# Kernel tuning notes

Measured on AMD Instinct MI355X. Metric: run time of the kernel, lower is better.

The kernel has to match this reference:

```python
import jax, jax.numpy as jnp
import numpy as np

HEADS, DIM_HEAD, DIM = 12, 64, 768
H = W = 32
N = H * W
B = 4


def _ln(x, g, b, eps=1e-5):
    mu = x.mean(-1, keepdims=True)
    var = ((x - mu) ** 2).mean(-1, keepdims=True)
    return (x - mu) / jnp.sqrt(var + eps) * g + b


def _get_epipolar(k, src_c2w, target_c2w, h=H, w=W):
    # Faithful port of Epipolar_Attention.get_epipolar, without the (hw*hw,3) repeat
    # materialization (uses broadcasting for the pairwise cross product instead).
    b = k.shape[0]
    Wf = h * 16.0 / 9.0
    k = k.astype(jnp.float32)
    k = k.at[:, 0, :].multiply(Wf).at[:, 1, :].multiply(float(h))
    k = k.at[:, 0, 2].set(h / 2.0).at[:, 1, 2].set(h / 2.0)
    ii, jj = jnp.meshgrid(jnp.arange(h), jnp.arange(w), indexing='ij')
    # after the torch column swap: (col, row, 1)
    coords = jnp.stack([jj.ravel(), ii.ravel(), jnp.ones(h * w, jnp.int32)], axis=1).astype(jnp.float32)  # [hw,3]
    k3 = k[:, :3, :3]
    src_r, src_t = src_c2w[:, :3, :3].astype(jnp.float32), src_c2w[:, :3, 3].astype(jnp.float32)
    tgt_r, tgt_t = target_c2w[:, :3, :3].astype(jnp.float32), target_c2w[:, :3, 3].astype(jnp.float32)
    tgt_rinv = jnp.linalg.inv(tgt_r)
    fx, fy = k3[:, 0, 0][:, None], k3[:, 1, 1][:, None]
    cx, cy = k3[:, 0, 2][:, None], k3[:, 1, 2][:, None]
    nc = jnp.stack([(coords[None, :, 0] - cx) / fx,
                    (coords[None, :, 1] - cy) / fy,
                    jnp.broadcast_to(coords[None, :, 2], (b, h * w))], axis=-1)  # [b,hw,3]
    p3w = jnp.einsum('bij,bnj->bni', src_r, nc) + src_t[:, None]
    p2 = jnp.einsum('bij,bnj->bni', tgt_rinv, p3w) - tgt_t[:, None]  # target_w2c_t = -target_c2w_t
    pij_un = jnp.einsum('bij,bnj->bni', k3, p2)                      # [b,hw,3]
    pij = pij_un / (pij_un[..., -1:] + 1e-6)
    o2 = jnp.einsum('bij,bj->bi', tgt_rinv, src_t) - tgt_t           # origin projected
    oij = jnp.einsum('bij,bj->bi', k3, o2)
    oij = oij / oij[..., -1:]
    oi_to_pi = pij - oij[:, None]                # [b,hw,3]
    oi_to_coord = coords[None] - oij[:, None]    # [b,hw,3]
    cr = jnp.cross(oi_to_pi[:, :, None, :], oi_to_coord[:, None, :, :])  # [b,hw,hw,3]
    area = jnp.sqrt((cr * cr).sum(-1))
    vlen = jnp.sqrt((oi_to_pi * oi_to_pi).sum(-1))[:, :, None]
    dist = area / vlen
    dw = 1.0 - jax.nn.sigmoid(50.0 * (dist - 0.5))
    row_max = dw.max(-1, keepdims=True)
    return jnp.where(row_max < 0.5, 1.0, dw)     # rows with max<0.5 are set to all-ones


def setup_inputs():
    key = jax.random.key(0)
    ks = jax.random.split(key, 16)
    s = 0.02
    x = jax.random.normal(ks[0], (B, N, DIM), jnp.float32)
    src_encode = jax.random.normal(ks[1], (B, N, DIM), jnp.float32)
    intrinsic = (jnp.zeros((B, 4, 4), jnp.float32)
                 .at[:, 0, 0].set(1.0).at[:, 1, 1].set(1.0)
                 .at[:, 0, 2].set(0.5).at[:, 1, 2].set(0.5)
                 .at[:, 2, 2].set(1.0).at[:, 3, 3].set(1.0))
    R = jnp.eye(3, dtype=jnp.float32) + 0.1 * jax.random.normal(ks[2], (2, B, 3, 3), jnp.float32)
    t = 0.5 * jax.random.normal(ks[3], (2, B, 3), jnp.float32)
    c2w = (jnp.zeros((2, B, 4, 4), jnp.float32)
           .at[:, :, :3, :3].set(R).at[:, :, :3, 3].set(t).at[:, :, 3, 3].set(1.0))
    hd = HEADS * DIM_HEAD
    w_ = lambda k_, shp: s * jax.random.normal(k_, shp, jnp.float32)
    return dict(
        x=x, src_encode=src_encode, intrinsic=intrinsic, c2w=c2w,
        lnq_g=jnp.ones(DIM), lnq_b=jnp.zeros(DIM), Wq=w_(ks[4], (DIM, hd)), bq=jnp.zeros(hd),
        lnk_g=jnp.ones(DIM), lnk_b=jnp.zeros(DIM), Wk=w_(ks[5], (DIM, hd)), bk=jnp.zeros(hd),
        lnv_g=jnp.ones(DIM), lnv_b=jnp.zeros(DIM), Wv=w_(ks[6], (DIM, hd)), bv=jnp.zeros(hd),
        Wp=w_(ks[7], (hd, DIM)), bp=jnp.zeros(DIM),
        pre_g=jnp.ones(DIM), pre_b=jnp.zeros(DIM),
        W1=w_(ks[8], (DIM, 2 * DIM)), b1=jnp.zeros(2 * DIM),
        W2=w_(ks[9], (2 * DIM, DIM)), b2=jnp.zeros(DIM),
        post_g=jnp.ones(DIM), post_b=jnp.zeros(DIM))


def reference(x, src_encode, intrinsic, c2w, lnq_g, lnq_b, Wq, bq, lnk_g, lnk_b, Wk, bk,
              lnv_g, lnv_b, Wv, bv, Wp, bp, pre_g, pre_b, W1, b1, W2, b2, post_g, post_b):
    b, n, _ = x.shape
    scale = DIM_HEAD ** -0.5
    split = lambda t_: t_.reshape(b, n, HEADS, DIM_HEAD).transpose(0, 2, 1, 3)  # [b,m,n,d]
    q = split(_ln(x, lnq_g, lnq_b) @ Wq + bq)
    k = split(_ln(src_encode, lnk_g, lnk_b) @ Wk + bk)
    v = split(_ln(src_encode, lnv_g, lnv_b) @ Wv + bv)
    scores = scale * jnp.einsum('bmqd,bmkd->bmqk', q, k)
    e1 = _get_epipolar(intrinsic, c2w[1], c2w[0])                    # do_epipolar
    e2 = jnp.swapaxes(_get_epipolar(intrinsic, c2w[0], c2w[1]), 1, 2)  # bidirectional (transposed)
    wmap = e1 * e2                                                   # [b,n,n], shared across heads
    att = jax.nn.softmax(scores * wmap[:, None], axis=-1)
    a = jnp.einsum('bmqk,bmkd->bmqd', att, v).transpose(0, 2, 1, 3).reshape(b, n, HEADS * DIM_HEAD)
    z = _ln(a @ Wp + bp, pre_g, pre_b)
    z = z + (jax.nn.gelu(z @ W1 + b1, approximate=False) @ W2 + b2)  # torch nn.GELU = exact erf
    z = _ln(z, post_g, post_b)
    wm_full = jnp.broadcast_to(wmap[:, None], (b, HEADS, n, n)).reshape(b * HEADS, n, n)
    return z, wm_full
```

## Files before the change

kernel.cpp:

```cpp
#include <hip/hip_runtime.h>
#include <hip/hip_bf16.h>

typedef unsigned short u16;
typedef __attribute__((ext_vector_type(4))) unsigned short u16x4;
typedef __attribute__((ext_vector_type(8))) unsigned short u16x8;
typedef __attribute__((ext_vector_type(8))) short s16x8;
typedef __attribute__((ext_vector_type(4))) float f32x4;

#define HEADS 12
#define NSEQ 1024
#define DIMM 768
#define DHEAD 64

__device__ __forceinline__ float b2f(u16 h) {
  union { unsigned u; float f; } v; v.u = ((unsigned)h) << 16; return v.f;
}
__device__ __forceinline__ u16 f2b(float f) {
  union { float f; unsigned u; } v; v.f = f;
  unsigned r = v.u + 0x7fffu + ((v.u >> 16) & 1u);
  return (u16)(r >> 16);
}
__device__ __forceinline__ void gl_lds16(const u16* g, u16* l) {
  __builtin_amdgcn_global_load_lds(
      (const __attribute__((address_space(1))) void*)g,
      (__attribute__((address_space(3))) void*)l, 16, 0, 0);
}

template<bool GELU, bool RESID>
__device__ __forceinline__ void gemm_body(
    const u16* __restrict__ A, const u16* __restrict__ BT,
    const float* __restrict__ bias, const u16* __restrict__ resid,
    const float* __restrict__ rg, const float* __restrict__ rb,
    u16* __restrict__ C, int K, int lda, int ldb, int ldc,
    int m0, int n0, u16* As, u16* Bs)
{
  const int tid = threadIdx.x;
  const int lane = tid & 63;
  const int wv = tid >> 6;
  const int wm0 = (wv >> 1) * 64;
  const int wn0 = (wv & 1) * 64;
  const int l15 = lane & 15;
  const int quad = lane >> 4;
  const int srow = lane >> 2;
  const int scol = (lane & 3) * 8;

  f32x4 acc[4][4];
  #pragma unroll
  for (int i = 0; i < 4; ++i)
    #pragma unroll
    for (int j = 0; j < 4; ++j)
      acc[i][j] = {0.f, 0.f, 0.f, 0.f};

  const u16* Ab = A + (long)(m0 + wv * 32 + srow) * lda + scol;
  const u16* Bb = BT + (long)(n0 + wv * 32 + srow) * ldb + scol;
  u16* AsW = As + (wv * 32) * 32;
  u16* BsW = Bs + (wv * 32) * 32;

  #pragma unroll
  for (int t = 0; t < 2; ++t) {
    gl_lds16(Ab + (long)t * 16 * lda, AsW + t * 16 * 32);
    gl_lds16(Bb + (long)t * 16 * ldb, BsW + t * 16 * 32);
  }

  int cur = 0;
  for (int k0 = 0; k0 < K; k0 += 32) {
    __syncthreads();
    if (k0 + 32 < K) {
      const int nxt = cur ^ 1;
      #pragma unroll
      for (int t = 0; t < 2; ++t) {
        gl_lds16(Ab + (k0 + 32) + (long)t * 16 * lda, AsW + nxt * 4096 + t * 16 * 32);
        gl_lds16(Bb + (k0 + 32) + (long)t * 16 * ldb, BsW + nxt * 4096 + t * 16 * 32);
      }
    }
    const u16* Ac = As + cur * 4096;
    const u16* Bc = Bs + cur * 4096;
    s16x8 af[4], bfr[4];
    #pragma unroll
    for (int i = 0; i < 4; ++i)
      af[i] = *(const s16x8*)&Ac[(wm0 + i * 16 + l15) * 32 + quad * 8];
    #pragma unroll
    for (int j = 0; j < 4; ++j)
      bfr[j] = *(const s16x8*)&Bc[(wn0 + j * 16 + l15) * 32 + quad * 8];
    #pragma unroll
    for (int i = 0; i < 4; ++i)
      #pragma unroll
      for (int j = 0; j < 4; ++j)
        acc[i][j] = __builtin_amdgcn_mfma_f32_16x16x32_bf16(af[i], bfr[j], acc[i][j], 0, 0, 0);
    cur ^= 1;
  }

  #pragma unroll
  for (int i = 0; i < 4; ++i)
    #pragma unroll
    for (int j = 0; j < 4; ++j) {
      const int col = n0 + wn0 + j * 16 + l15;
      const float bvv = bias[col];
      #pragma unroll
      for (int v = 0; v < 4; ++v) {
        const int row = m0 + wm0 + i * 16 + quad * 4 + v;
        float val = acc[i][j][v] + bvv;
        if (GELU) val = 0.5f * val * (1.0f + erff(val * 0.70710678118654752440f));
        if (RESID) val += b2f(resid[(long)row * ldc + col]) * rg[col] + rb[col];
        C[(long)row * ldc + col] = f2b(val);
      }
    }
}

template<bool GELU, bool RESID>
__global__ __launch_bounds__(256)
void gemm_one(const u16* __restrict__ A, const u16* __restrict__ BT,
              const float* __restrict__ bias, const u16* __restrict__ resid,
              const float* __restrict__ rg, const float* __restrict__ rb,
              u16* __restrict__ C, int K, int lda, int ldb, int ldc)
{
  __shared__ u16 As[8192], Bs[8192];
  gemm_body<GELU, RESID>(A, BT, bias, resid, rg, rb, C, K, lda, ldb, ldc,
                         blockIdx.x * 128, blockIdx.y * 128, As, Bs);
}

__global__ __launch_bounds__(256)
void gemm_qkv(const u16* __restrict__ nx, const u16* __restrict__ ns,
              const u16* __restrict__ qT, const u16* __restrict__ kvT,
              const float* __restrict__ bqf, const float* __restrict__ bkvf,
              u16* __restrict__ qb, u16* __restrict__ kvb)
{
  __shared__ u16 As[8192], Bs[8192];
  const int z = blockIdx.z;
  if (z == 0)
    gemm_body<false, false>(nx, qT, bqf, nullptr, nullptr, nullptr, qb,
                            768, 768, 768, 768,
                            blockIdx.x * 128, blockIdx.y * 128, As, Bs);
  else
    gemm_body<false, false>(ns, kvT, bkvf, nullptr, nullptr, nullptr, kvb,
                            768, 768, 768, 1536,
                            blockIdx.x * 128, (z - 1) * 768 + blockIdx.y * 128, As, Bs);
}

__global__ __launch_bounds__(256, 3)
void fattn(const u16* __restrict__ qb, const u16* __restrict__ kvb,
           const u16* __restrict__ vT, const u16* __restrict__ wm,
           u16* __restrict__ outA)
{
  __shared__ u16 Qs[2 * 64 * 32];
  __shared__ u16 Ks[2 * 64 * 32];
  __shared__ u16 Vs[2 * 64 * 32];
  __shared__ u16 Ws[64][72];
  __shared__ u16 Ps[64][72];

  const int bh = blockIdx.y;
  const int b = bh / HEADS, h = bh - b * HEADS;
  const int q0 = blockIdx.x * 64;
  const int tid = threadIdx.x;
  const int lane = tid & 63;
  const int wv = tid >> 6;
  const int l15 = lane & 15;
  const int quad = lane >> 4;
  const int srow = lane >> 2;
  const int scol = (lane & 3) * 8;

  const u16* Qg = qb + ((long)b * NSEQ + q0) * DIMM + h * DHEAD;
  const u16* Kg = kvb + (long)b * NSEQ * 1536 + h * DHEAD;
  const u16* Vg = vT + (long)bh * DHEAD * NSEQ;
  const u16* Wg = wm + ((long)b * NSEQ + q0) * NSEQ;

  #pragma unroll
  for (int h2 = 0; h2 < 2; ++h2)
    gl_lds16(Qg + (long)(wv * 16 + srow) * DIMM + h2 * 32 + scol,
             Qs + (h2 * 64 + wv * 16) * 32);

  f32x4 Sacc[4], Oacc[4];
  float mrow[4], lrow[4];
  #pragma unroll
  for (int j = 0; j < 4; ++j) {
    Oacc[j] = {0.f, 0.f, 0.f, 0.f};
    mrow[j] = -3.0e38f;
    lrow[j] = 0.f;
  }
  s16x8 qf[2];

  for (int kt = 0; kt < 16; ++kt) {
    __syncthreads();
    #pragma unroll
    for (int h2 = 0; h2 < 2; ++h2) {
      gl_lds16(Kg + (long)(kt * 64 + wv * 16 + srow) * 1536 + h2 * 32 + scol,
               Ks + (h2 * 64 + wv * 16) * 32);
      gl_lds16(Vg + (long)(wv * 16 + srow) * NSEQ + kt * 64 + h2 * 32 + scol,
               Vs + (h2 * 64 + wv * 16) * 32);
    }
    #pragma unroll
    for (int t = 0; t < 2; ++t) {
      const int col = (lane & 3) * 16 + t * 8;
      u16x8 wvv = *(const u16x8*)&Wg[(long)(wv * 16 + srow) * NSEQ + kt * 64 + col];
      *(u16x8*)&Ws[wv * 16 + srow][col] = wvv;
    }
    __syncthreads();

    if (kt == 0) {
      qf[0] = *(const s16x8*)&Qs[(0 * 64 + wv * 16 + l15) * 32 + quad * 8];
      qf[1] = *(const s16x8*)&Qs[(1 * 64 + wv * 16 + l15) * 32 + quad * 8];
    }

    #pragma unroll
    for (int j = 0; j < 4; ++j) Sacc[j] = {0.f, 0.f, 0.f, 0.f};
    #pragma unroll
    for (int j = 0; j < 4; ++j)
      #pragma unroll
      for (int h2 = 0; h2 < 2; ++h2) {
        s16x8 kf = *(const s16x8*)&Ks[(h2 * 64 + j * 16 + l15) * 32 + quad * 8];
        Sacc[j] = __builtin_amdgcn_mfma_f32_16x16x32_bf16(qf[h2], kf, Sacc[j], 0, 0, 0);
      }

    #pragma unroll
    for (int j = 0; j < 4; ++j)
      #pragma unroll
      for (int v = 0; v < 4; ++v)
        Sacc[j][v] *= b2f(Ws[wv * 16 + quad * 4 + v][j * 16 + l15]);
    #pragma unroll
    for (int v = 0; v < 4; ++v) {
      float tm = fmaxf(fmaxf(Sacc[0][v], Sacc[1][v]), fmaxf(Sacc[2][v], Sacc[3][v]));
      tm = fmaxf(tm, __shfl_xor(tm, 1));
      tm = fmaxf(tm, __shfl_xor(tm, 2));
      tm = fmaxf(tm, __shfl_xor(tm, 4));
      tm = fmaxf(tm, __shfl_xor(tm, 8));
      const float mnew = fmaxf(mrow[v], tm);
      const float al = __expf(mrow[v] - mnew);
      float rs = 0.f;
      #pragma unroll
      for (int j = 0; j < 4; ++j) {
        const float e = __expf(Sacc[j][v] - mnew);
        Sacc[j][v] = e;
        rs += e;
      }
      rs += __shfl_xor(rs, 1);
      rs += __shfl_xor(rs, 2);
      rs += __shfl_xor(rs, 4);
      rs += __shfl_xor(rs, 8);
      lrow[v] = lrow[v] * al + rs;
      mrow[v] = mnew;
      #pragma unroll
      for (int jn = 0; jn < 4; ++jn) Oacc[jn][v] *= al;
    }
    #pragma unroll
    for (int j = 0; j < 4; ++j)
      #pragma unroll
      for (int v = 0; v < 4; ++v)
        Ps[wv * 16 + quad * 4 + v][j * 16 + l15] = f2b(Sacc[j][v]);

    #pragma unroll
    for (int h2 = 0; h2 < 2; ++h2) {
      s16x8 af = *(const s16x8*)&Ps[wv * 16 + l15][h2 * 32 + quad * 8];
      #pragma unroll
      for (int jn = 0; jn < 4; ++jn) {
        s16x8 vf = *(const s16x8*)&Vs[(h2 * 64 + jn * 16 + l15) * 32 + quad * 8];
        Oacc[jn] = __builtin_amdgcn_mfma_f32_16x16x32_bf16(af, vf, Oacc[jn], 0, 0, 0);
      }
    }
  }

  #pragma unroll
  for (int v = 0; v < 4; ++v) {
    const int row = q0 + wv * 16 + quad * 4 + v;
    const float inv = 1.0f / lrow[v];
    #pragma unroll
    for (int jn = 0; jn < 4; ++jn)
      outA[((long)(b * NSEQ + row)) * DIMM + h * DHEAD + jn * 16 + l15] =
          f2b(Oacc[jn][v] * inv);
  }
}

template<bool F32IN>
__global__ __launch_bounds__(256)
void norm_k(const void* __restrict__ in, u16* __restrict__ out)
{
  const long base = (long)blockIdx.x * DIMM;
  const int tid = threadIdx.x;
  __shared__ float s1[8], s2[8];
  float v0, v1, v2;
  if (F32IN) {
    const float* p = (const float*)in + base;
    v0 = p[tid]; v1 = p[tid + 256]; v2 = p[tid + 512];
  } else {
    const u16* p = (const u16*)in + base;
    v0 = b2f(p[tid]); v1 = b2f(p[tid + 256]); v2 = b2f(p[tid + 512]);
  }
  float s = v0 + v1 + v2;
  #pragma unroll
  for (int off = 32; off; off >>= 1) s += __shfl_down(s, off);
  const int lane = tid & 63, wid = tid >> 6;
  if (!lane) s1[wid] = s;
  __syncthreads();
  if (!tid) s1[4] = s1[0] + s1[1] + s1[2] + s1[3];
  __syncthreads();
  const float mu = s1[4] / 768.0f;
  float d0 = v0 - mu, d1 = v1 - mu, d2 = v2 - mu;
  float sq = d0 * d0 + d1 * d1 + d2 * d2;
  #pragma unroll
  for (int off = 32; off; off >>= 1) sq += __shfl_down(sq, off);
  if (!lane) s2[wid] = sq;
  __syncthreads();
  if (!tid) s2[4] = s2[0] + s2[1] + s2[2] + s2[3];
  __syncthreads();
  const float rstd = 1.0f / sqrtf(s2[4] / 768.0f + 1e-5f);
  u16* o = out + base;
  o[tid]       = f2b(d0 * rstd);
  o[tid + 256] = f2b(d1 * rstd);
  o[tid + 512] = f2b(d2 * rstd);
}

__global__ __launch_bounds__(256)
void ln_final(const u16* __restrict__ in, const float* __restrict__ g,
              const float* __restrict__ bb, float* __restrict__ out)
{
  const long base = (long)blockIdx.x * DIMM;
  const int tid = threadIdx.x;
  __shared__ float s1[8], s2[8];
  const u16* p = in + base;
  float v0 = b2f(p[tid]), v1 = b2f(p[tid + 256]), v2 = b2f(p[tid + 512]);
  float s = v0 + v1 + v2;
  #pragma unroll
  for (int off = 32; off; off >>= 1) s += __shfl_down(s, off);
  const int lane = tid & 63, wid = tid >> 6;
  if (!lane) s1[wid] = s;
  __syncthreads();
  if (!tid) s1[4] = s1[0] + s1[1] + s1[2] + s1[3];
  __syncthreads();
  const float mu = s1[4] / 768.0f;
  float d0 = v0 - mu, d1 = v1 - mu, d2 = v2 - mu;
  float sq = d0 * d0 + d1 * d1 + d2 * d2;
  #pragma unroll
  for (int off = 32; off; off >>= 1) sq += __shfl_down(sq, off);
  if (!lane) s2[wid] = sq;
  __syncthreads();
  if (!tid) s2[4] = s2[0] + s2[1] + s2[2] + s2[3];
  __syncthreads();
  const float rstd = 1.0f / sqrtf(s2[4] / 768.0f + 1e-5f);
  float* o = out + base;
  o[tid]       = d0 * rstd * g[tid]       + bb[tid];
  o[tid + 256] = d1 * rstd * g[tid + 256] + bb[tid + 256];
  o[tid + 512] = d2 * rstd * g[tid + 512] + bb[tid + 512];
}

__global__ __launch_bounds__(256)
void trans_all(const float* w0, const float* w1, const float* w2,
               const float* w3, const float* w4, const float* w5,
               const float* gq, const float* gk, const float* gv, const float* gp,
               u16* d0, u16* d12, u16* d3, u16* d4, u16* d5)
{
  const float* src; const float* g; u16* dst; int R, C; float sc = 1.0f;
  switch (blockIdx.z) {
    case 0: src = w0; g = gq; dst = d0;  R = 768;  C = 768;  sc = 0.125f; break;
    case 1: src = w1; g = gk; dst = d12; R = 768;  C = 768;  break;
    case 2: src = w2; g = gv; dst = d12 + 768 * 768; R = 768; C = 768; break;
    case 3: src = w3; g = nullptr; dst = d3; R = 768;  C = 768;  break;
    case 4: src = w4; g = gp; dst = d4; R = 768;  C = 1536; break;
    default: src = w5; g = nullptr; dst = d5; R = 1536; C = 768; break;
  }
  const int c0 = blockIdx.x * 32;
  const int r0 = blockIdx.y * 32;
  if (c0 >= C || r0 >= R) return;
  __shared__ u16 t[32][36];
  const int tid = threadIdx.x;
  const int i = tid >> 3;
  const int j4 = (tid & 7) * 4;
  const float rs = (g ? g[r0 + i] : 1.0f) * sc;
  #pragma unroll
  for (int jj = 0; jj < 4; ++jj)
    t[i][j4 + jj] = f2b(src[(long)(r0 + i) * C + c0 + j4 + jj] * rs);
  __syncthreads();
  u16x4 ov;
  #pragma unroll
  for (int jj = 0; jj < 4; ++jj) ov[jj] = t[j4 + jj][i];
  *(u16x4*)&dst[(long)(c0 + i) * R + r0 + j4] = ov;
}

__global__ __launch_bounds__(256)
void biasfold(const float* Wq, const float* Wk, const float* Wv, const float* W1,
              const float* bq, const float* bk, const float* bv, const float* b1,
              const float* lnqb, const float* lnkb, const float* lnvb, const float* preb,
              float* obq, float* obkv, float* ob1)
{
  const int y = blockIdx.y;
  const int c = blockIdx.x * 256 + threadIdx.x;
  const float* W; const float* bln; const float* bw; float* out;
  int C; float sc = 1.0f;
  switch (y) {
    case 0: W = Wq; bln = lnqb; bw = bq; out = obq;        C = 768;  sc = 0.125f; break;
    case 1: W = Wk; bln = lnkb; bw = bk; out = obkv;       C = 768;  break;
    case 2: W = Wv; bln = lnvb; bw = bv; out = obkv + 768; C = 768;  break;
    default: W = W1; bln = preb; bw = b1; out = ob1;       C = 1536; break;
  }
  if (c >= C) return;
  float s = bw[c];
  for (int r = 0; r < 768; ++r) s += bln[r] * W[(long)r * C + c];
  out[c] = s * sc;
}

__global__ __launch_bounds__(256)
void v_transpose(const u16* __restrict__ kvb, u16* __restrict__ vT)
{
  __shared__ u16 t[64][72];
  const int z = blockIdx.y;
  const int b = z / HEADS, h = z - b * HEADS;
  const int n0 = blockIdx.x * 64;
  const int tid = threadIdx.x;
  const int i = tid >> 2;
  const int jb = (tid & 3) * 16;
  const u16* src = kvb + (long)(b * NSEQ + n0 + i) * 1536 + 768 + h * DHEAD + jb;
  *(u16x8*)&t[i][jb]     = *(const u16x8*)&src[0];
  *(u16x8*)&t[i][jb + 8] = *(const u16x8*)&src[8];
  __syncthreads();
  const int dd = tid >> 2;
  const int nb = (tid & 3) * 16;
  u16x8 o0, o1;
  #pragma unroll
  for (int nn = 0; nn < 8; ++nn) { o0[nn] = t[nb + nn][dd]; o1[nn] = t[nb + 8 + nn][dd]; }
  u16* dst = vT + ((long)z * DHEAD + dd) * NSEQ + n0 + nb;
  *(u16x8*)&dst[0] = o0;
  *(u16x8*)&dst[8] = o1;
}

__global__ void epi_setup(const float* __restrict__ intr, const float* __restrict__ c2w,
                          float* __restrict__ u4, float* __restrict__ oijb)
{
  const int db = blockIdx.x;
  const int d = db >> 2, b = db & 3;
  __shared__ float S[36];
  if (threadIdx.x == 0) {
    const int sidx = (d == 0) ? 1 : 0;
    const int tidx = 1 - sidx;
    float k3[9], sr[9], st[3], tr[9], tt[3];
    const float Wf = 32.0f * 16.0f / 9.0f;
    for (int j = 0; j < 3; ++j) {
      k3[j]     = intr[(b * 4 + 0) * 4 + j] * Wf;
      k3[3 + j] = intr[(b * 4 + 1) * 4 + j] * 32.0f;
      k3[6 + j] = intr[(b * 4 + 2) * 4 + j];
    }
    k3[2] = 16.0f; k3[5] = 16.0f;
    for (int i = 0; i < 3; ++i) {
      for (int j = 0; j < 3; ++j) {
        sr[i * 3 + j] = c2w[((sidx * 4 + b) * 4 + i) * 4 + j];
        tr[i * 3 + j] = c2w[((tidx * 4 + b) * 4 + i) * 4 + j];
      }
      st[i] = c2w[((sidx * 4 + b) * 4 + i) * 4 + 3];
      tt[i] = c2w[((tidx * 4 + b) * 4 + i) * 4 + 3];
    }
    double a = tr[0], bb_ = tr[1], c = tr[2];
    double dd2 = tr[3], e = tr[4], f = tr[5];
    double g2 = tr[6], h2 = tr[7], i2 = tr[8];
    double det = a * (e * i2 - f * h2) - bb_ * (dd2 * i2 - f * g2) + c * (dd2 * h2 - e * g2);
    double inv[9] = {
      (e * i2 - f * h2), (c * h2 - bb_ * i2), (bb_ * f - c * e),
      (f * g2 - dd2 * i2), (a * i2 - c * g2), (c * dd2 - a * f),
      (dd2 * h2 - e * g2), (bb_ * g2 - a * h2), (a * e - bb_ * dd2)
    };
    float tri[9];
    for (int t2 = 0; t2 < 9; ++t2) tri[t2] = (float)(inv[t2] / det);
    float o2[3], oij[3];
    for (int i3 = 0; i3 < 3; ++i3)
      o2[i3] = tri[i3 * 3] * st[0] + tri[i3 * 3 + 1] * st[1] + tri[i3 * 3 + 2] * st[2] - tt[i3];
    for (int i3 = 0; i3 < 3; ++i3)
      oij[i3] = k3[i3 * 3] * o2[0] + k3[i3 * 3 + 1] * o2[1] + k3[i3 * 3 + 2] * o2[2];
    const float ozf = oij[2];
    oij[0] = oij[0] / ozf; oij[1] = oij[1] / ozf; oij[2] = ozf / ozf;
    for (int t2 = 0; t2 < 9; ++t2) { S[t2] = k3[t2]; S[9 + t2] = sr[t2]; S[21 + t2] = tri[t2]; }
    for (int t2 = 0; t2 < 3; ++t2) { S[18 + t2] = st[t2]; S[30 + t2] = tt[t2]; S[33 + t2] = oij[t2]; }
    oijb[db * 4 + 0] = oij[0]; oijb[db * 4 + 1] = oij[1]; oijb[db * 4 + 2] = oij[2];
    oijb[db * 4 + 3] = 0.f;
  }
  __syncthreads();
  for (int n = threadIdx.x; n < 1024; n += blockDim.x) {
    const float ncx = ((float)(n & 31) - S[2]) / S[0];
    const float ncy = ((float)(n >> 5) - S[5]) / S[4];
    const float p0 = S[9]  * ncx + S[10] * ncy + S[11] + S[18];
    const float p1 = S[12] * ncx + S[13] * ncy + S[14] + S[19];
    const float p2 = S[15] * ncx + S[16] * ncy + S[17] + S[20];
    const float q0 = S[21] * p0 + S[22] * p1 + S[23] * p2 - S[30];
    const float q1 = S[24] * p0 + S[25] * p1 + S[26] * p2 - S[31];
    const float q2 = S[27] * p0 + S[28] * p1 + S[29] * p2 - S[32];
    const float w0 = S[0] * q0 + S[1] * q1 + S[2] * q2;
    const float w1 = S[3] * q0 + S[4] * q1 + S[5] * q2;
    const float w2 = S[6] * q0 + S[7] * q1 + S[8] * q2;
    const float pz = w2 + 1e-6f;
    const float ux = w0 / pz - S[33];
    const float uy = w1 / pz - S[34];
    const float uz = w2 / pz - S[35];
    const float vlen = sqrtf(ux * ux + uy * uy + uz * uz);
    f32x4 uo = {ux, uy, uz, vlen};
    *(f32x4*)&u4[((long)db * 1024 + n) * 4] = uo;
  }
}

__global__ __launch_bounds__(256)
void epi_dw(const float* __restrict__ u4, const float* __restrict__ oijb,
            float* __restrict__ dw)
{
  const int rowid = blockIdx.x;
  const int db = rowid >> 10;
  const f32x4 U = *(const f32x4*)&u4[(long)rowid * 4];
  const float ox = oijb[db * 4 + 0];
  const float oy = oijb[db * 4 + 1];
  const float oz = oijb[db * 4 + 2];
  const int tid = threadIdx.x;
  __shared__ float red[8];
  float vals[4];
  float mx = -1e30f;
  #pragma unroll
  for (int i = 0; i < 4; ++i) {
    const int m = tid + i * 256;
    const float cx = (float)(m & 31) - ox;
    const float cy = (float)(m >> 5) - oy;
    const float cz = 1.0f - oz;
    const float crx = U.y * cz - U.z * cy;
    const float cry = U.z * cx - U.x * cz;
    const float crz = U.x * cy - U.y * cx;
    const float area = sqrtf(crx * crx + cry * cry + crz * crz);
    const float dist = area / U.w;
    const float t = 50.0f * (dist - 0.5f);
    const float dwv = 1.0f - 1.0f / (1.0f + __expf(-t));
    vals[i] = dwv;
    mx = fmaxf(mx, dwv);
  }
  #pragma unroll
  for (int off = 32; off; off >>= 1) mx = fmaxf(mx, __shfl_down(mx, off));
  const int lane = tid & 63, wid = tid >> 6;
  if (!lane) red[wid] = mx;
  __syncthreads();
  if (!tid) red[4] = fmaxf(fmaxf(red[0], red[1]), fmaxf(red[2], red[3]));
  __syncthreads();
  const bool fill1 = red[4] < 0.5f;
  float* out = dw + (long)rowid * 1024;
  #pragma unroll
  for (int i = 0; i < 4; ++i)
    out[tid + i * 256] = fill1 ? 1.0f : vals[i];
}

__global__ __launch_bounds__(256)
void epi_wmap(const float* __restrict__ dw, u16* __restrict__ wm,
              float* __restrict__ wm_full)
{
  __shared__ float tb[32][33];
  const int b = blockIdx.z;
  const int q0 = blockIdx.x * 32;
  const int k0 = blockIdx.y * 32;
  const int tid = threadIdx.x;
  const int i = tid >> 3;
  const int j4 = (tid & 7) * 4;
  const float* d1 = dw + ((long)(4 + b) * 1024 + (k0 + i)) * 1024 + q0 + j4;
  #pragma unroll
  for (int jj = 0; jj < 4; ++jj) tb[i][j4 + jj] = d1[jj];
  __syncthreads();
  const float* d0 = dw + ((long)b * 1024 + (q0 + i)) * 1024 + k0 + j4;
  u16x4 pk;
  f32x4 wf;
  #pragma unroll
  for (int jj = 0; jj < 4; ++jj) {
    const float w = d0[jj] * tb[j4 + jj][i];
    wf[jj] = w;
    pk[jj] = f2b(w);
  }
  *(u16x4*)&wm[((long)b * 1024 + q0 + i) * 1024 + k0 + j4] = pk;
  #pragma unroll
  for (int h = 0; h < HEADS; ++h)
    *(f32x4*)&wm_full[((long)(b * HEADS + h) * 1024 + q0 + i) * 1024 + k0 + j4] = wf;
}

extern "C" void kernel_launch(void* const* d_in, const int* in_sizes, int n_in,
                              void* d_out, int out_size, void* d_ws, size_t ws_size,
                              hipStream_t stream)
{
  (void)in_sizes; (void)n_in; (void)out_size; (void)ws_size;
  const float* x     = (const float*)d_in[0];
  const float* src   = (const float*)d_in[1];
  const float* intr  = (const float*)d_in[2];
  const float* c2w   = (const float*)d_in[3];
  const float* lnq_g = (const float*)d_in[4];
  const float* lnq_b = (const float*)d_in[5];
  const float* Wq    = (const float*)d_in[6];
  const float* bq    = (const float*)d_in[7];
  const float* lnk_g = (const float*)d_in[8];
  const float* lnk_b = (const float*)d_in[9];
  const float* Wk    = (const float*)d_in[10];
  const float* bk    = (const float*)d_in[11];
  const float* lnv_g = (const float*)d_in[12];
  const float* lnv_b = (const float*)d_in[13];
  const float* Wv    = (const float*)d_in[14];
  const float* bv    = (const float*)d_in[15];
  const float* Wp    = (const float*)d_in[16];
  const float* bp    = (const float*)d_in[17];
  const float* pre_g = (const float*)d_in[18];
  const float* pre_b = (const float*)d_in[19];
  const float* W1    = (const float*)d_in[20];
  const float* b1    = (const float*)d_in[21];
  const float* W2    = (const float*)d_in[22];
  const float* b2    = (const float*)d_in[23];
  const float* post_g= (const float*)d_in[24];
  const float* post_b= (const float*)d_in[25];

  char* ws = (char*)d_ws;
  size_t off = 0;
  auto alloc = [&](size_t bytes) -> char* {
    char* p = ws + off;
    off = (off + bytes + 255) & ~(size_t)255;
    return p;
  };
  const size_t SEQD = (size_t)4096 * 768 * 2;

  u16* WqT  = (u16*)alloc(768 * 768 * 2);
  u16* WkvT = (u16*)alloc((size_t)1536 * 768 * 2);
  u16* WpT  = (u16*)alloc(768 * 768 * 2);
  u16* W1T  = (u16*)alloc(768 * 1536 * 2);
  u16* W2T  = (u16*)alloc(1536 * 768 * 2);
  float* bqf  = (float*)alloc(768 * 4);
  float* bkvf = (float*)alloc(1536 * 4);
  float* b1f  = (float*)alloc(1536 * 4);
  char* pool = alloc(6 * SEQD);
  float* u4   = (float*)alloc(8 * 1024 * 4 * 4);
  float* oijb = (float*)alloc(8 * 4 * 4);
  u16* wmapb  = (u16*)alloc((size_t)4 * 1024 * 1024 * 2);
  float* dwbuf = (float*)alloc((size_t)8 * 1024 * 1024 * 4);

  u16* S0 = (u16*)pool;
  u16* S1 = (u16*)(pool + SEQD);
  u16* S2 = (u16*)(pool + 2 * SEQD);
  u16* S3 = (u16*)(pool + 3 * SEQD);
  u16* S5 = (u16*)(pool + 5 * SEQD);

  float* out_z  = (float*)d_out;
  float* out_wm = (float*)d_out + (size_t)4 * 1024 * 768;

  trans_all<<<dim3(48, 48, 6), 256, 0, stream>>>(
      Wq, Wk, Wv, Wp, W1, W2, lnq_g, lnk_g, lnv_g, pre_g,
      WqT, WkvT, WpT, W1T, W2T);
  biasfold<<<dim3(6, 4), 256, 0, stream>>>(
      Wq, Wk, Wv, W1, bq, bk, bv, b1, lnq_b, lnk_b, lnv_b, pre_b,
      bqf, bkvf, b1f);

  epi_setup<<<8, 128, 0, stream>>>(intr, c2w, u4, oijb);
  epi_dw<<<8192, 256, 0, stream>>>(u4, oijb, dwbuf);
  epi_wmap<<<dim3(32, 32, 4), 256, 0, stream>>>(dwbuf, wmapb, out_wm);

  norm_k<true><<<4096, 256, 0, stream>>>(x, S0);
  norm_k<true><<<4096, 256, 0, stream>>>(src, S1);

  gemm_qkv<<<dim3(32, 6, 3), 256, 0, stream>>>(S0, S1, WqT, WkvT, bqf, bkvf, S2, S3);

  v_transpose<<<dim3(16, 48), 256, 0, stream>>>(S3, S5);

  fattn<<<dim3(16, 48), 256, 0, stream>>>(S2, S3, S5, wmapb, S0);

  gemm_one<false, false><<<dim3(32, 6), 256, 0, stream>>>(
      S0, WpT, bp, nullptr, nullptr, nullptr, S1, 768, 768, 768, 768);

  norm_k<false><<<4096, 256, 0, stream>>>(S1, S2);

  gemm_one<true, false><<<dim3(32, 12), 256, 0, stream>>>(
      S2, W1T, b1f, nullptr, nullptr, nullptr, S3, 768, 768, 768, 1536);

  gemm_one<false, true><<<dim3(32, 6), 256, 0, stream>>>(
      S3, W2T, b2, S2, pre_g, pre_b, S5, 1536, 1536, 1536, 768);

  ln_final<<<4096, 256, 0, stream>>>(S5, post_g, post_b, out_z);
}
```

Before: 560.6 us.

## Recompute epipolar weights in wmap, double-buffer attention, shrink GEMM tiles, fuse norms

The epipolar path no longer writes a full 32MB float distance buffer. A flags kernel keeps only the per-row fill flag, and epi_wmap recomputes both directional weights inline. The attention kernel double-buffers K/V tiles in LDS and reads the weight map straight from global into registers, which removes one barrier per tile. The output GEMMs switch to 128x64 tiles with double buffering for more blocks, and the two input layernorms merge into one launch. The cost is extra recompute of the sigmoid and more LDS per attention block, which may lower occupancy.

Result: faster. 518.7 us (-7.5%).

```diff
diff --git a/kernel.cpp b/kernel.cpp
--- a/kernel.cpp
+++ b/kernel.cpp
@@ -108,15 +108,93 @@
 }
 
 template<bool GELU, bool RESID>
+__device__ __forceinline__ void gemm_body64(
+    const u16* __restrict__ A, const u16* __restrict__ BT,
+    const float* __restrict__ bias, const u16* __restrict__ resid,
+    const float* __restrict__ rg, const float* __restrict__ rb,
+    u16* __restrict__ C, int K, int lda, int ldb, int ldc,
+    int m0, int n0, u16* As, u16* Bs)
+{
+  const int tid = threadIdx.x;
+  const int lane = tid & 63;
+  const int wv = tid >> 6;
+  const int wm0 = wv * 32;
+  const int l15 = lane & 15;
+  const int quad = lane >> 4;
+  const int srow = lane >> 2;
+  const int scol = (lane & 3) * 8;
+
+  f32x4 acc[2][4];
+  #pragma unroll
+  for (int i = 0; i < 2; ++i)
+    #pragma unroll
+    for (int j = 0; j < 4; ++j)
+      acc[i][j] = {0.f, 0.f, 0.f, 0.f};
+
+  const u16* Ab = A + (long)(m0 + wv * 32 + srow) * lda + scol;
+  const u16* Bb = BT + (long)(n0 + wv * 16 + srow) * ldb + scol;
+  u16* AsW = As + (wv * 32) * 32;
+  u16* BsW = Bs + (wv * 16) * 32;
+
+  #pragma unroll
+  for (int t = 0; t < 2; ++t)
+    gl_lds16(Ab + (long)t * 16 * lda, AsW + t * 16 * 32);
+  gl_lds16(Bb, BsW);
+
+  int cur = 0;
+  for (int k0 = 0; k0 < K; k0 += 32) {
+    __syncthreads();
+    if (k0 + 32 < K) {
+      const int nxt = cur ^ 1;
+      #pragma unroll
+      for (int t = 0; t < 2; ++t)
+        gl_lds16(Ab + (k0 + 32) + (long)t * 16 * lda, AsW + nxt * 4096 + t * 16 * 32);
+      gl_lds16(Bb + (k0 + 32), BsW + nxt * 2048);
+    }
+    const u16* Ac = As + cur * 4096;
+    const u16* Bc = Bs + cur * 2048;
+    s16x8 af[2], bfr[4];
+    #pragma unroll
+    for (int i = 0; i < 2; ++i)
+      af[i] = *(const s16x8*)&Ac[(wm0 + i * 16 + l15) * 32 + quad * 8];
+    #pragma unroll
+    for (int j = 0; j < 4; ++j)
+      bfr[j] = *(const s16x8*)&Bc[(j * 16 + l15) * 32 + quad * 8];
+    #pragma unroll
+    for (int i = 0; i < 2; ++i)
+      #pragma unroll
+      for (int j = 0; j < 4; ++j)
+        acc[i][j] = __builtin_amdgcn_mfma_f32_16x16x32_bf16(af[i], bfr[j], acc[i][j], 0, 0, 0);
+    cur ^= 1;
+  }
+
+  #pragma unroll
+  for (int i = 0; i < 2; ++i)
+    #pragma unroll
+    for (int j = 0; j < 4; ++j) {
+      const int col = n0 + j * 16 + l15;
+      const float bvv = bias[col];
+      #pragma unroll
+      for (int v = 0; v < 4; ++v) {
+        const int row = m0 + wm0 + i * 16 + quad * 4 + v;
+        float val = acc[i][j][v] + bvv;
+        if (GELU) val = 0.5f * val * (1.0f + erff(val * 0.70710678118654752440f));
+        if (RESID) val += b2f(resid[(long)row * ldc + col]) * rg[col] + rb[col];
+        C[(long)row * ldc + col] = f2b(val);
+      }
+    }
+}
+
+template<bool GELU, bool RESID>
 __global__ __launch_bounds__(256)
 void gemm_one(const u16* __restrict__ A, const u16* __restrict__ BT,
               const float* __restrict__ bias, const u16* __restrict__ resid,
               const float* __restrict__ rg, const float* __restrict__ rb,
               u16* __restrict__ C, int K, int lda, int ldb, int ldc)
 {
-  __shared__ u16 As[8192], Bs[8192];
-  gemm_body<GELU, RESID>(A, BT, bias, resid, rg, rb, C, K, lda, ldb, ldc,
-                         blockIdx.x * 128, blockIdx.y * 128, As, Bs);
+  __shared__ u16 As[8192], Bs[4096];
+  gemm_body64<GELU, RESID>(A, BT, bias, resid, rg, rb, C, K, lda, ldb, ldc,
+                           blockIdx.x * 128, blockIdx.y * 64, As, Bs);
 }
 
 __global__ __launch_bounds__(256)
@@ -143,9 +221,8 @@
            u16* __restrict__ outA)
 {
   __shared__ u16 Qs[2 * 64 * 32];
-  __shared__ u16 Ks[2 * 64 * 32];
-  __shared__ u16 Vs[2 * 64 * 32];
-  __shared__ u16 Ws[64][72];
+  __shared__ u16 Ks[2][2 * 64 * 32];
+  __shared__ u16 Vs[2][2 * 64 * 32];
   __shared__ u16 Ps[64][72];
 
   const int bh = blockIdx.y;
@@ -165,9 +242,14 @@
   const u16* Wg = wm + ((long)b * NSEQ + q0) * NSEQ;
 
   #pragma unroll
-  for (int h2 = 0; h2 < 2; ++h2)
+  for (int h2 = 0; h2 < 2; ++h2) {
     gl_lds16(Qg + (long)(wv * 16 + srow) * DIMM + h2 * 32 + scol,
              Qs + (h2 * 64 + wv * 16) * 32);
+    gl_lds16(Kg + (long)(wv * 16 + srow) * 1536 + h2 * 32 + scol,
+             Ks[0] + (h2 * 64 + wv * 16) * 32);
+    gl_lds16(Vg + (long)(wv * 16 + srow) * NSEQ + h2 * 32 + scol,
+             Vs[0] + (h2 * 64 + wv * 16) * 32);
+  }
 
   f32x4 Sacc[4], Oacc[4];
   float mrow[4], lrow[4];
@@ -179,35 +261,39 @@
   }
   s16x8 qf[2];
 
+  int cur = 0;
   for (int kt = 0; kt < 16; ++kt) {
     __syncthreads();
-    #pragma unroll
-    for (int h2 = 0; h2 < 2; ++h2) {
-      gl_lds16(Kg + (long)(kt * 64 + wv * 16 + srow) * 1536 + h2 * 32 + scol,
-               Ks + (h2 * 64 + wv * 16) * 32);
-      gl_lds16(Vg + (long)(wv * 16 + srow) * NSEQ + kt * 64 + h2 * 32 + scol,
-               Vs + (h2 * 64 + wv * 16) * 32);
-    }
-    #pragma unroll
-    for (int t = 0; t < 2; ++t) {
-      const int col = (lane & 3) * 16 + t * 8;
-      u16x8 wvv = *(const u16x8*)&Wg[(long)(wv * 16 + srow) * NSEQ + kt * 64 + col];
-      *(u16x8*)&Ws[wv * 16 + srow][col] = wvv;
-    }
-    __syncthreads();
+    if (kt < 15) {
+      const int nxt = cur ^ 1;
+      #pragma unroll
+      for (int h2 = 0; h2 < 2; ++h2) {
+        gl_lds16(Kg + (long)((kt + 1) * 64 + wv * 16 + srow) * 1536 + h2 * 32 + scol,
+                 Ks[nxt] + (h2 * 64 + wv * 16) * 32);
+        gl_lds16(Vg + (long)(wv * 16 + srow) * NSEQ + (kt + 1) * 64 + h2 * 32 + scol,
+                 Vs[nxt] + (h2 * 64 + wv * 16) * 32);
+      }
+    }
 
     if (kt == 0) {
       qf[0] = *(const s16x8*)&Qs[(0 * 64 + wv * 16 + l15) * 32 + quad * 8];
       qf[1] = *(const s16x8*)&Qs[(1 * 64 + wv * 16 + l15) * 32 + quad * 8];
     }
 
+    float wr[4][4];
+    #pragma unroll
+    for (int j = 0; j < 4; ++j)
+      #pragma unroll
+      for (int v = 0; v < 4; ++v)
+        wr[j][v] = b2f(Wg[(long)(wv * 16 + quad * 4 + v) * NSEQ + kt * 64 + j * 16 + l15]);
+
     #pragma unroll
     for (int j = 0; j < 4; ++j) Sacc[j] = {0.f, 0.f, 0.f, 0.f};
     #pragma unroll
     for (int j = 0; j < 4; ++j)
       #pragma unroll
       for (int h2 = 0; h2 < 2; ++h2) {
-        s16x8 kf = *(const s16x8*)&Ks[(h2 * 64 + j * 16 + l15) * 32 + quad * 8];
+        s16x8 kf = *(const s16x8*)&Ks[cur][(h2 * 64 + j * 16 + l15) * 32 + quad * 8];
         Sacc[j] = __builtin_amdgcn_mfma_f32_16x16x32_bf16(qf[h2], kf, Sacc[j], 0, 0, 0);
       }
 
@@ -215,7 +301,7 @@
     for (int j = 0; j < 4; ++j)
       #pragma unroll
       for (int v = 0; v < 4; ++v)
-        Sacc[j][v] *= b2f(Ws[wv * 16 + quad * 4 + v][j * 16 + l15]);
+        Sacc[j][v] *= wr[j][v];
     #pragma unroll
     for (int v = 0; v < 4; ++v) {
       float tm = fmaxf(fmaxf(Sacc[0][v], Sacc[1][v]), fmaxf(Sacc[2][v], Sacc[3][v]));
@@ -252,10 +338,11 @@
       s16x8 af = *(const s16x8*)&Ps[wv * 16 + l15][h2 * 32 + quad * 8];
       #pragma unroll
       for (int jn = 0; jn < 4; ++jn) {
-        s16x8 vf = *(const s16x8*)&Vs[(h2 * 64 + jn * 16 + l15) * 32 + quad * 8];
+        s16x8 vf = *(const s16x8*)&Vs[cur][(h2 * 64 + jn * 16 + l15) * 32 + quad * 8];
         Oacc[jn] = __builtin_amdgcn_mfma_f32_16x16x32_bf16(af, vf, Oacc[jn], 0, 0, 0);
       }
     }
+    cur ^= 1;
   }
 
   #pragma unroll
@@ -303,6 +390,39 @@
   __syncthreads();
   const float rstd = 1.0f / sqrtf(s2[4] / 768.0f + 1e-5f);
   u16* o = out + base;
+  o[tid]       = f2b(d0 * rstd);
+  o[tid + 256] = f2b(d1 * rstd);
+  o[tid + 512] = f2b(d2 * rstd);
+}
+
+__global__ __launch_bounds__(256)
+void norm_dual(const float* __restrict__ inA, const float* __restrict__ inB,
+               u16* __restrict__ outA, u16* __restrict__ outB)
+{
+  const int r = blockIdx.x;
+  const float* p = ((r < 4096) ? inA : inB) + (long)(r & 4095) * DIMM;
+  u16* o = ((r < 4096) ? outA : outB) + (long)(r & 4095) * DIMM;
+  const int tid = threadIdx.x;
+  __shared__ float s1[8], s2[8];
+  float v0 = p[tid], v1 = p[tid + 256], v2 = p[tid + 512];
+  float s = v0 + v1 + v2;
+  #pragma unroll
+  for (int off = 32; off; off >>= 1) s += __shfl_down(s, off);
+  const int lane = tid & 63, wid = tid >> 6;
+  if (!lane) s1[wid] = s;
+  __syncthreads();
+  if (!tid) s1[4] = s1[0] + s1[1] + s1[2] + s1[3];
+  __syncthreads();
+  const float mu = s1[4] / 768.0f;
+  float d0 = v0 - mu, d1 = v1 - mu, d2 = v2 - mu;
+  float sq = d0 * d0 + d1 * d1 + d2 * d2;
+  #pragma unroll
+  for (int off = 32; off; off >>= 1) sq += __shfl_down(sq, off);
+  if (!lane) s2[wid] = sq;
+  __syncthreads();
+  if (!tid) s2[4] = s2[0] + s2[1] + s2[2] + s2[3];
+  __syncthreads();
+  const float rstd = 1.0f / sqrtf(s2[4] / 768.0f + 1e-5f);
   o[tid]       = f2b(d0 * rstd);
   o[tid + 256] = f2b(d1 * rstd);
   o[tid + 512] = f2b(d2 * rstd);
@@ -491,9 +611,23 @@
   }
 }
 
-__global__ __launch_bounds__(256)
-void epi_dw(const float* __restrict__ u4, const float* __restrict__ oijb,
-            float* __restrict__ dw)
+__device__ __forceinline__ float dwval(f32x4 U, float ox, float oy, float oz, int m)
+{
+  const float cx = (float)(m & 31) - ox;
+  const float cy = (float)(m >> 5) - oy;
+  const float cz = 1.0f - oz;
+  const float crx = U.y * cz - U.z * cy;
+  const float cry = U.z * cx - U.x * cz;
+  const float crz = U.x * cy - U.y * cx;
+  const float area = sqrtf(crx * crx + cry * cry + crz * crz);
+  const float dist = area / U.w;
+  const float t = 50.0f * (dist - 0.5f);
+  return 1.0f - 1.0f / (1.0f + __expf(-t));
+}
+
+__global__ __launch_bounds__(256)
+void epi_flags(const float* __restrict__ u4, const float* __restrict__ oijb,
+               float* __restrict__ flags)
 {
   const int rowid = blockIdx.x;
   const int db = rowid >> 10;
@@ -503,59 +637,57 @@
   const float oz = oijb[db * 4 + 2];
   const int tid = threadIdx.x;
   __shared__ float red[8];
-  float vals[4];
   float mx = -1e30f;
   #pragma unroll
-  for (int i = 0; i < 4; ++i) {
-    const int m = tid + i * 256;
-    const float cx = (float)(m & 31) - ox;
-    const float cy = (float)(m >> 5) - oy;
-    const float cz = 1.0f - oz;
-    const float crx = U.y * cz - U.z * cy;
-    const float cry = U.z * cx - U.x * cz;
-    const float crz = U.x * cy - U.y * cx;
-    const float area = sqrtf(crx * crx + cry * cry + crz * crz);
-    const float dist = area / U.w;
-    const float t = 50.0f * (dist - 0.5f);
-    const float dwv = 1.0f - 1.0f / (1.0f + __expf(-t));
-    vals[i] = dwv;
-    mx = fmaxf(mx, dwv);
-  }
+  for (int i = 0; i < 4; ++i)
+    mx = fmaxf(mx, dwval(U, ox, oy, oz, tid + i * 256));
   #pragma unroll
   for (int off = 32; off; off >>= 1) mx = fmaxf(mx, __shfl_down(mx, off));
   const int lane = tid & 63, wid = tid >> 6;
   if (!lane) red[wid] = mx;
   __syncthreads();
-  if (!tid) red[4] = fmaxf(fmaxf(red[0], red[1]), fmaxf(red[2], red[3]));
-  __syncthreads();
-  const bool fill1 = red[4] < 0.5f;
-  float* out = dw + (long)rowid * 1024;
-  #pragma unroll
-  for (int i = 0; i < 4; ++i)
-    out[tid + i * 256] = fill1 ? 1.0f : vals[i];
-}
-
-__global__ __launch_bounds__(256)
-void epi_wmap(const float* __restrict__ dw, u16* __restrict__ wm,
-              float* __restrict__ wm_full)
-{
-  __shared__ float tb[32][33];
+  if (!tid) {
+    const float m4 = fmaxf(fmaxf(red[0], red[1]), fmaxf(red[2], red[3]));
+    flags[rowid] = (m4 < 0.5f) ? 1.0f : 0.0f;
+  }
+}
+
+__global__ __launch_bounds__(256)
+void epi_wmap(const float* __restrict__ u4, const float* __restrict__ oijb,
+              const float* __restrict__ flags,
+              u16* __restrict__ wm, float* __restrict__ wm_full)
+{
   const int b = blockIdx.z;
   const int q0 = blockIdx.x * 32;
   const int k0 = blockIdx.y * 32;
   const int tid = threadIdx.x;
   const int i = tid >> 3;
   const int j4 = (tid & 7) * 4;
-  const float* d1 = dw + ((long)(4 + b) * 1024 + (k0 + i)) * 1024 + q0 + j4;
-  #pragma unroll
-  for (int jj = 0; jj < 4; ++jj) tb[i][j4 + jj] = d1[jj];
-  __syncthreads();
-  const float* d0 = dw + ((long)b * 1024 + (q0 + i)) * 1024 + k0 + j4;
+
+  __shared__ f32x4 U2s[32];
+  __shared__ float f2s[32];
+  __shared__ float f1s[32];
+  if (tid < 32) {
+    U2s[tid] = *(const f32x4*)&u4[((long)(4 + b) * 1024 + k0 + tid) * 4];
+    f2s[tid] = flags[(4 + b) * 1024 + k0 + tid];
+    f1s[tid] = flags[b * 1024 + q0 + tid];
+  }
+  __syncthreads();
+
+  const int q = q0 + i;
+  const f32x4 U1 = *(const f32x4*)&u4[((long)b * 1024 + q) * 4];
+  const float o1x = oijb[b * 4 + 0], o1y = oijb[b * 4 + 1], o1z = oijb[b * 4 + 2];
+  const float o2x = oijb[(4 + b) * 4 + 0], o2y = oijb[(4 + b) * 4 + 1], o2z = oijb[(4 + b) * 4 + 2];
+  const bool fl1 = f1s[i] > 0.5f;
+
   u16x4 pk;
   f32x4 wf;
   #pragma unroll
   for (int jj = 0; jj < 4; ++jj) {
-    const float w = d0[jj] * tb[j4 + jj][i];
+    const int k = k0 + j4 + jj;
+    const float e1 = fl1 ? 1.0f : dwval(U1, o1x, o1y, o1z, k);
+    const float e2 = (f2s[j4 + jj] > 0.5f) ? 1.0f : dwval(U2s[j4 + jj], o2x, o2y, o2z, q);
+    const float w = e1 * e2;
     wf[jj] = w;
     pk[jj] = f2b(w);
   }
@@ -618,7 +750,7 @@
   float* u4   = (float*)alloc(8 * 1024 * 4 * 4);
   float* oijb = (float*)alloc(8 * 4 * 4);
   u16* wmapb  = (u16*)alloc((size_t)4 * 1024 * 1024 * 2);
-  float* dwbuf = (float*)alloc((size_t)8 * 1024 * 1024 * 4);
+  float* flagb = (float*)alloc(8 * 1024 * 4);
 
   u16* S0 = (u16*)pool;
   u16* S1 = (u16*)(pool + SEQD);
@@ -637,11 +769,10 @@
       bqf, bkvf, b1f);
 
   epi_setup<<<8, 128, 0, stream>>>(intr, c2w, u4, oijb);
-  epi_dw<<<8192, 256, 0, stream>>>(u4, oijb, dwbuf);
-  epi_wmap<<<dim3(32, 32, 4), 256, 0, stream>>>(dwbuf, wmapb, out_wm);
-
-  norm_k<true><<<4096, 256, 0, stream>>>(x, S0);
-  norm_k<true><<<4096, 256, 0, stream>>>(src, S1);
+  epi_flags<<<8192, 256, 0, stream>>>(u4, oijb, flagb);
+  epi_wmap<<<dim3(32, 32, 4), 256, 0, stream>>>(u4, oijb, flagb, wmapb, out_wm);
+
+  norm_dual<<<8192, 256, 0, stream>>>(x, src, S0, S1);
 
   gemm_qkv<<<dim3(32, 6, 3), 256, 0, stream>>>(S0, S1, WqT, WkvT, bqf, bkvf, S2, S3);
 
@@ -649,15 +780,15 @@
 
   fattn<<<dim3(16, 48), 256, 0, stream>>>(S2, S3, S5, wmapb, S0);
 
-  gemm_one<false, false><<<dim3(32, 6), 256, 0, stream>>>(
+  gemm_one<false, false><<<dim3(32, 12), 256, 0, stream>>>(
       S0, WpT, bp, nullptr, nullptr, nullptr, S1, 768, 768, 768, 768);
 
   norm_k<false><<<4096, 256, 0, stream>>>(S1, S2);
 
-  gemm_one<true, false><<<dim3(32, 12), 256, 0, stream>>>(
+  gemm_one<true, false><<<dim3(32, 24), 256, 0, stream>>>(
       S2, W1T, b1f, nullptr, nullptr, nullptr, S3, 768, 768, 768, 1536);
 
-  gemm_one<false, true><<<dim3(32, 6), 256, 0, stream>>>(
+  gemm_one<false, true><<<dim3(32, 12), 256, 0, stream>>>(
       S3, W2T, b2, S2, pre_g, pre_b, S5, 1536, 1536, 1536, 768);
 
   ln_final<<<4096, 256, 0, stream>>>(S5, post_g, post_b, out_z);
```
